# Optimization experiments

Measured on AMD Instinct MI355X. Metric: run time of the kernel, lower is better.

The kernel has to match this reference:

```python
import jax, jax.numpy as jnp
import numpy as np

NEG_SLOPE = 0.2

def _gat_conv(x, src, dst, W, a_src, a_dst, b, heads, out_ch, concat):
    N = x.shape[0]
    h = (x @ W).reshape(N, heads, out_ch)                      # [N,H,C]
    al_s = jnp.einsum('nhc,hc->nh', h, a_src)                  # [N,H]
    al_d = jnp.einsum('nhc,hc->nh', h, a_dst)
    e = jax.nn.leaky_relu(al_s[src] + al_d[dst], NEG_SLOPE)    # [E,H]
    emax = jax.ops.segment_max(e, dst, num_segments=N)         # [N,H]
    ex = jnp.exp(e - emax[dst])
    denom = jax.ops.segment_sum(ex, dst, num_segments=N)
    alpha = ex / denom[dst]                                    # [E,H]
    msg = h[src] * alpha[:, :, None]                           # [E,H,C]
    out = jax.ops.segment_sum(msg, dst, num_segments=N)        # [N,H,C]
    if concat:
        out = out.reshape(N, heads * out_ch)
    else:
        out = out.mean(axis=1)
    return out + b

def _add_self_loops(edge_index, N):
    loops = jnp.arange(N, dtype=edge_index.dtype)
    src = jnp.concatenate([edge_index[0], loops])
    dst = jnp.concatenate([edge_index[1], loops])
    return src, dst

def setup_inputs() -> dict:
    key = jax.random.key(0)
    ks = jax.random.split(key, 16)
    N, E, Fin, C, H, G, OUT = 50000, 1600000, 128, 32, 8, 256, 64
    s = 0.05
    inp = {
        'x': jax.random.normal(ks[0], (N, Fin), jnp.float32),
        'edge_index': jax.random.randint(ks[1], (2, E), 0, N, jnp.int64),
        'batch': jnp.sort(jax.random.randint(ks[2], (N,), 0, G, jnp.int64)),
        'W0': jax.random.normal(ks[3], (Fin, H * C), jnp.float32) * s,
        'a_src0': jax.random.normal(ks[4], (H, C), jnp.float32) * s,
        'a_dst0': jax.random.normal(ks[5], (H, C), jnp.float32) * s,
        'b0': jnp.zeros((H * C,), jnp.float32),
        'W1': jax.random.normal(ks[6], (H * C, H * C), jnp.float32) * s,
        'a_src1': jax.random.normal(ks[7], (H, C), jnp.float32) * s,
        'a_dst1': jax.random.normal(ks[8], (H, C), jnp.float32) * s,
        'b1': jnp.zeros((H * C,), jnp.float32),
        'W2': jax.random.normal(ks[9], (H * C, C), jnp.float32) * s,
        'a_src2': jax.random.normal(ks[10], (1, C), jnp.float32) * s,
        'a_dst2': jax.random.normal(ks[11], (1, C), jnp.float32) * s,
        'b2': jnp.zeros((C,), jnp.float32),
        'lin_w': jax.random.normal(ks[12], (C, OUT), jnp.float32) * s,
        'lin_b': jnp.zeros((OUT,), jnp.float32),
    }
    return inp

def reference(x, edge_index, batch, W0, a_src0, a_dst0, b0, W1, a_src1, a_dst1, b1,
              W2, a_src2, a_dst2, b2, lin_w, lin_b):
    N = x.shape[0]
    G = 256
    src, dst = _add_self_loops(edge_index, N)
    h = jax.nn.relu(_gat_conv(x, src, dst, W0, a_src0, a_dst0, b0, 8, 32, True))
    h = jax.nn.relu(_gat_conv(h, src, dst, W1, a_src1, a_dst1, b1, 8, 32, True))
    h = _gat_conv(h, src, dst, W2, a_src2, a_dst2, b2, 1, 32, True)  # heads=1 concat -> [N,32]
    # global mean pool over graphs
    sums = jax.ops.segment_sum(h, batch, num_segments=G)
    cnts = jax.ops.segment_sum(jnp.ones((N,), h.dtype), batch, num_segments=G)
    pooled = sums / jnp.maximum(cnts, 1.0)[:, None]
    return pooled @ lin_w + lin_b
```

## Files before the change

kernel.cpp:

```cpp
#include <hip/hip_runtime.h>
#include <hip/hip_bf16.h>


#define LRELU(x) ((x) >= 0.f ? (x) : 0.2f * (x))

typedef unsigned short ushort8 __attribute__((ext_vector_type(8)));
typedef unsigned short ushort4v __attribute__((ext_vector_type(4)));
typedef __attribute__((ext_vector_type(8))) short bf16x8;
typedef __attribute__((ext_vector_type(4))) float f32x4;

__device__ __forceinline__ float bf2f(unsigned short u) {
    return __uint_as_float(((unsigned)u) << 16);
}
__device__ __forceinline__ unsigned short f2bf(float f) {
    __hip_bfloat16 b = __float2bfloat16(f);
    return *reinterpret_cast<unsigned short*>(&b);
}
__device__ __forceinline__ void gl_lds16(const unsigned short* g, unsigned short* l) {
    __builtin_amdgcn_global_load_lds((const __attribute__((address_space(1))) void*)g,
                                     (__attribute__((address_space(3))) void*)l, 16, 0, 0);
}


template <int BM, int BN, int WM, int WN, int H>
__device__ __forceinline__
void gemm_core(unsigned short* __restrict__ Ab, unsigned short* __restrict__ Bb,
               const unsigned short* __restrict__ A, const unsigned short* __restrict__ Bt,
               unsigned short* __restrict__ Cc,
               const float* __restrict__ a_src, const float* __restrict__ a_dst,
               float* __restrict__ als, float* __restrict__ ald,
               int M, int Nn, int K, int bxi, int byi) {
    constexpr int BK = 64;
    constexpr int MT = WM / 16, NT = WN / 16;
    constexpr int NWX = BN / WN;
    constexpr int NHL = WN / 32;
    const int tid = threadIdx.x;
    const int lane = tid & 63;
    const int wave = tid >> 6;
    const int wx = wave % NWX, wy = wave / NWX;
    const int by = byi * BM;
    const int bx = bxi * BN;
    const int r16 = lane & 15, kg = lane >> 4;
    const int srow = lane >> 3, sslot = lane & 7;

    f32x4 acc[MT][NT];
#pragma unroll
    for (int i = 0; i < MT; i++)
#pragma unroll
        for (int j = 0; j < NT; j++) acc[i][j] = (f32x4){0.f, 0.f, 0.f, 0.f};

    for (int k0 = 0; k0 < K; k0 += BK) {
        for (int t = wave; t < BM / 8; t += 4) {
            int gm = by + t * 8 + srow;
            if (gm >= M) gm = M - 1;
            gl_lds16(A + (size_t)gm * K + k0 + sslot * 8, Ab + (t * 8) * BK);
        }
        for (int t = wave; t < BN / 8; t += 4) {
            int gn = bx + t * 8 + srow;
            gl_lds16(Bt + (size_t)gn * K + k0 + sslot * 8, Bb + (t * 8) * BK);
        }
        __syncthreads();
#pragma unroll
        for (int ks = 0; ks < 2; ks++) {
            bf16x8 bh[NT];
#pragma unroll
            for (int j = 0; j < NT; j++)
                bh[j] = *(const bf16x8*)(Bb + (wx * WN + j * 16 + r16) * BK + ks * 32 + kg * 8);
#pragma unroll
            for (int i = 0; i < MT; i++) {
                bf16x8 ah = *(const bf16x8*)(Ab + (wy * WM + i * 16 + r16) * BK + ks * 32 + kg * 8);
#pragma unroll
                for (int j = 0; j < NT; j++)
                    acc[i][j] = __builtin_amdgcn_mfma_f32_16x16x32_bf16(ah, bh[j], acc[i][j], 0, 0, 0);
            }
        }
        __syncthreads();
    }

    const int c0 = bx + wx * WN;
#pragma unroll
    for (int i = 0; i < MT; i++) {
#pragma unroll
        for (int r = 0; r < 4; r++) {
            int gm = by + wy * WM + i * 16 + kg * 4 + r;
            bool ok = gm < M;
            float sa[NHL] = {};
            float sd[NHL] = {};
#pragma unroll
            for (int j = 0; j < NT; j++) {
                int gn = c0 + j * 16 + r16;
                float v = acc[i][j][r];
                if (ok) Cc[(size_t)gm * Nn + gn] = f2bf(v);
                sa[j >> 1] += v * a_src[gn];
                sd[j >> 1] += v * a_dst[gn];
            }
#pragma unroll
            for (int m = 1; m < 16; m <<= 1) {
#pragma unroll
                for (int t = 0; t < NHL; t++) {
                    sa[t] += __shfl_xor(sa[t], m);
                    sd[t] += __shfl_xor(sd[t], m);
                }
            }
            if (ok && r16 == 0) {
#pragma unroll
                for (int t = 0; t < NHL; t++) {
                    int hh = (c0 >> 5) + t;
                    als[(size_t)gm * H + hh] = sa[t];
                    ald[(size_t)gm * H + hh] = sd[t];
                }
            }
        }
    }
}


__global__ __launch_bounds__(256)
void deg_prep_kernel(const int* __restrict__ dst, int* __restrict__ deg, int E, int N,
                     const float* __restrict__ x, const float* __restrict__ W0,
                     const float* __restrict__ W1, const float* __restrict__ W2,
                     unsigned short* __restrict__ xb, unsigned short* __restrict__ w0t,
                     unsigned short* __restrict__ w1t, unsigned short* __restrict__ w2t,
                     int DEG_BLKS) {
    if ((int)blockIdx.x < DEG_BLKS) {
        int i = blockIdx.x * 256 + threadIdx.x;
        if (i < E) atomicAdd(&deg[dst[i]], 1);
        else if (i < E + N) atomicAdd(&deg[i - E], 1);
        return;
    }
    int i = (blockIdx.x - DEG_BLKS) * 256 + threadIdx.x;
    int nx = N * 128;
    if (i < nx) { xb[i] = f2bf(x[i]); return; }
    i -= nx;
    if (i < 256 * 128) {
        int n = i / 128, k = i - n * 128;
        w0t[i] = f2bf(W0[(size_t)k * 256 + n]);
        return;
    }
    i -= 256 * 128;
    if (i < 256 * 256) {
        int n = i / 256, k = i - n * 256;
        w1t[i] = f2bf(W1[(size_t)k * 256 + n]);
        return;
    }
    i -= 256 * 256;
    if (i < 32 * 256) {
        int n = i / 256, k = i - n * 256;
        w2t[i] = f2bf(W2[(size_t)k * 32 + n]);
    }
}


__global__ void scan_kernel(const int* __restrict__ deg, int* __restrict__ rowptr, int n,
                            const int* __restrict__ batch, int* __restrict__ gstart,
                            int N, int G) {
    const int tid = threadIdx.x;
    if (tid <= G) {
        int lo = 0, hi = N;
        while (lo < hi) { int mid = (lo + hi) >> 1; if (batch[mid] < tid) lo = mid + 1; else hi = mid; }
        gstart[tid] = lo;
    }
    __shared__ int partial[1024];
    const int chunk = (n + 1023) / 1024;
    const int start = min(tid * chunk, n);
    const int end = min(start + chunk, n);
    int s = 0;
    for (int i = start; i < end; i++) s += deg[i];
    partial[tid] = s;
    __syncthreads();
    for (int o = 1; o < 1024; o <<= 1) {
        int v = (tid >= o) ? partial[tid - o] : 0;
        __syncthreads();
        partial[tid] += v;
        __syncthreads();
    }
    int run = (tid == 0) ? 0 : partial[tid - 1];
    for (int i = start; i < end; i++) { rowptr[i] = run; run += deg[i]; }
    if (tid == 0) rowptr[n] = partial[1023];
}


__global__ __launch_bounds__(256)
void mega0_kernel(const unsigned short* __restrict__ A, const unsigned short* __restrict__ Bt,
                  unsigned short* __restrict__ Cc,
                  const float* __restrict__ a_src, const float* __restrict__ a_dst,
                  float* __restrict__ als, float* __restrict__ ald, int M, int K,
                  const int* __restrict__ src, const int* __restrict__ dst,
                  int* __restrict__ rowptr, int* __restrict__ col, int E, int N,
                  int GEMM_BLKS, int SCAT_BLKS) {
    __shared__ __attribute__((aligned(16))) unsigned short Ab[128 * 64];
    __shared__ __attribute__((aligned(16))) unsigned short Bb[128 * 64];
    const int bid = blockIdx.x;
    if (bid < GEMM_BLKS) {
        gemm_core<128, 128, 64, 64, 8>(Ab, Bb, A, Bt, Cc, a_src, a_dst, als, ald,
                                       M, 256, K, bid & 1, bid >> 1);
        return;
    }
    const int sb = bid - GEMM_BLKS;
    const int bin = sb / SCAT_BLKS;
    const int i = (sb - bin * SCAT_BLKS) * 256 + threadIdx.x;
    const int lo = (int)((long long)N * bin / 4);
    const int hi = (int)((long long)N * (bin + 1) / 4);
    int s, d;
    if (i < E) { d = dst[i]; s = src[i]; }
    else if (i < E + N) { d = i - E; s = d; }
    else return;
    if (d < lo || d >= hi) return;
    int pos = atomicAdd(&rowptr[d], 1);
    col[pos] = s;
}


template <int BM, int BN, int WM, int WN, int H>
__global__ __launch_bounds__(256)
void gemm_bf16_al(const unsigned short* __restrict__ A, const unsigned short* __restrict__ Bt,
                  unsigned short* __restrict__ Cc,
                  const float* __restrict__ a_src, const float* __restrict__ a_dst,
                  float* __restrict__ als, float* __restrict__ ald,
                  int M, int Nn, int K) {
    __shared__ __attribute__((aligned(16))) unsigned short Ab[BM * 64];
    __shared__ __attribute__((aligned(16))) unsigned short Bb[BN * 64];
    gemm_core<BM, BN, WM, WN, H>(Ab, Bb, A, Bt, Cc, a_src, a_dst, als, ald,
                                 M, Nn, K, blockIdx.x, blockIdx.y);
}


__global__ __launch_bounds__(256)
void gat_agg_w8(const unsigned short* __restrict__ hfeat,
                const float* __restrict__ als, const float* __restrict__ ald,
                const int* __restrict__ rowptr,
                const int* __restrict__ col,
                const float* __restrict__ bias,
                unsigned short* __restrict__ outH,
                int N) {
    constexpr int CAP = 128;
    const int wid = threadIdx.x >> 6;
    const int lane = threadIdx.x & 63;
    const int n = blockIdx.x * 4 + wid;
    __shared__ float se_all[4][CAP * 8];
    __shared__ int scol_all[4][CAP];
    if (n >= N) return;
    float* se = se_all[wid];
    int* scol = scol_all[wid];

    const int r0 = (n == 0) ? 0 : rowptr[n - 1];
    const int deg = rowptr[n] - r0;
    const int dcap = min(deg, CAP);

    for (int j = lane; j < dcap; j += 64) scol[j] = col[r0 + j];

    const int slot = lane >> 3, h = lane & 7;
    const float aldh = ald[(size_t)n * 8 + h];
    float psum = 0.f;
    for (int j = 0; j < deg; j += 8) {
        int e = j + slot;
        if (e < deg) {
            int s = (e < dcap) ? scol[e] : col[r0 + e];
            float ev = als[(size_t)s * 8 + h] + aldh;
            ev = LRELU(ev);
            float w = __expf(ev);
            psum += w;
            if (e < CAP) se[e * 8 + h] = w;
        }
    }
#pragma unroll
    for (int m = 8; m < 64; m <<= 1) psum += __shfl_xor(psum, m);
    const int q = lane >> 3;
    const float sinv = 1.0f / __shfl(psum, q);
    const float aldq = ald[(size_t)n * 8 + q];

    const int cb = lane * 4;
    float a0 = 0.f, a1 = 0.f, a2 = 0.f, a3 = 0.f;
    int j = 0;
    for (; j + 3 < dcap; j += 4) {
        int s0 = __builtin_amdgcn_readfirstlane(scol[j]);
        int s1 = __builtin_amdgcn_readfirstlane(scol[j + 1]);
        int s2 = __builtin_amdgcn_readfirstlane(scol[j + 2]);
        int s3 = __builtin_amdgcn_readfirstlane(scol[j + 3]);
        ushort4v v0 = *(const ushort4v*)(hfeat + (size_t)s0 * 256 + cb);
        ushort4v v1 = *(const ushort4v*)(hfeat + (size_t)s1 * 256 + cb);
        ushort4v v2 = *(const ushort4v*)(hfeat + (size_t)s2 * 256 + cb);
        ushort4v v3 = *(const ushort4v*)(hfeat + (size_t)s3 * 256 + cb);
        float w0 = se[j * 8 + q];
        float w1 = se[j * 8 + 8 + q];
        float w2 = se[j * 8 + 16 + q];
        float w3 = se[j * 8 + 24 + q];
        a0 += bf2f(v0[0]) * w0; a1 += bf2f(v0[1]) * w0; a2 += bf2f(v0[2]) * w0; a3 += bf2f(v0[3]) * w0;
        a0 += bf2f(v1[0]) * w1; a1 += bf2f(v1[1]) * w1; a2 += bf2f(v1[2]) * w1; a3 += bf2f(v1[3]) * w1;
        a0 += bf2f(v2[0]) * w2; a1 += bf2f(v2[1]) * w2; a2 += bf2f(v2[2]) * w2; a3 += bf2f(v2[3]) * w2;
        a0 += bf2f(v3[0]) * w3; a1 += bf2f(v3[1]) * w3; a2 += bf2f(v3[2]) * w3; a3 += bf2f(v3[3]) * w3;
    }
    for (; j < dcap; j++) {
        int s0 = __builtin_amdgcn_readfirstlane(scol[j]);
        ushort4v v0 = *(const ushort4v*)(hfeat + (size_t)s0 * 256 + cb);
        float w0 = se[j * 8 + q];
        a0 += bf2f(v0[0]) * w0; a1 += bf2f(v0[1]) * w0; a2 += bf2f(v0[2]) * w0; a3 += bf2f(v0[3]) * w0;
    }
    for (; j < deg; j++) {
        int s0 = col[r0 + j];
        float ev = als[(size_t)s0 * 8 + q] + aldq;
        ev = LRELU(ev);
        float w0 = __expf(ev);
        ushort4v v0 = *(const ushort4v*)(hfeat + (size_t)s0 * 256 + cb);
        a0 += bf2f(v0[0]) * w0; a1 += bf2f(v0[1]) * w0; a2 += bf2f(v0[2]) * w0; a3 += bf2f(v0[3]) * w0;
    }

    float4 b4 = *(const float4*)&bias[cb];
    float o0 = fmaxf(a0 * sinv + b4.x, 0.f);
    float o1 = fmaxf(a1 * sinv + b4.y, 0.f);
    float o2 = fmaxf(a2 * sinv + b4.z, 0.f);
    float o3 = fmaxf(a3 * sinv + b4.w, 0.f);
    const size_t ob = (size_t)n * 256 + cb;
    *(ushort4v*)&outH[ob] = (ushort4v){f2bf(o0), f2bf(o1), f2bf(o2), f2bf(o3)};
}


__global__ __launch_bounds__(256)
void gat_agg_h1w(const unsigned short* __restrict__ hfeat,
                 const float* __restrict__ als, const float* __restrict__ ald,
                 const int* __restrict__ rowptr, const int* __restrict__ col,
                 const float* __restrict__ bias, float* __restrict__ out, int N) {
    constexpr int CAP = 256;
    const int wid = threadIdx.x >> 6;
    const int lane = threadIdx.x & 63;
    const int n = blockIdx.x * 4 + wid;
    __shared__ float sw_all[4][CAP];
    __shared__ int scol_all[4][CAP];
    if (n >= N) return;
    float* sw = sw_all[wid];
    int* scol = scol_all[wid];

    const int r0 = (n == 0) ? 0 : rowptr[n - 1];
    const int deg = rowptr[n] - r0;
    const int dcap = min(deg, CAP);
    const float aldn = ald[n];

    float lsum = 0.f;
    for (int idx = lane; idx < deg; idx += 64) {
        int s = col[r0 + idx];
        float ev = als[s] + aldn;
        ev = LRELU(ev);
        float w = __expf(ev);
        if (idx < CAP) { sw[idx] = w; scol[idx] = s; }
        lsum += w;
    }
#pragma unroll
    for (int m = 1; m < 64; m <<= 1) lsum += __shfl_xor(lsum, m);
    const float sinv = 1.0f / lsum;

    const int slot = lane >> 3, ch = lane & 7;
    float a0 = 0.f, a1 = 0.f, a2 = 0.f, a3 = 0.f;
    for (int j = 0; j < dcap; j += 8) {
        int e = j + slot;
        int ec = min(e, dcap - 1);
        int s = scol[ec];
        float w = (e < dcap) ? sw[ec] : 0.f;
        ushort4v v = *(const ushort4v*)(hfeat + (size_t)s * 32 + ch * 4);
        a0 += bf2f(v[0]) * w; a1 += bf2f(v[1]) * w;
        a2 += bf2f(v[2]) * w; a3 += bf2f(v[3]) * w;
    }
    for (int j = CAP; j < deg; j += 8) {
        int e = j + slot;
        int ec = min(e, deg - 1);
        int s = col[r0 + ec];
        float w = 0.f;
        if (e < deg) {
            float ev = als[s] + aldn;
            ev = LRELU(ev);
            w = __expf(ev);
        }
        ushort4v v = *(const ushort4v*)(hfeat + (size_t)s * 32 + ch * 4);
        a0 += bf2f(v[0]) * w; a1 += bf2f(v[1]) * w;
        a2 += bf2f(v[2]) * w; a3 += bf2f(v[3]) * w;
    }
#pragma unroll
    for (int m = 8; m < 64; m <<= 1) {
        a0 += __shfl_xor(a0, m);
        a1 += __shfl_xor(a1, m);
        a2 += __shfl_xor(a2, m);
        a3 += __shfl_xor(a3, m);
    }
    if (slot == 0) {
        float4 b4 = *(const float4*)&bias[ch * 4];
        float4 o;
        o.x = a0 * sinv + b4.x;
        o.y = a1 * sinv + b4.y;
        o.z = a2 * sinv + b4.z;
        o.w = a3 * sinv + b4.w;
        *(float4*)&out[(size_t)n * 32 + ch * 4] = o;
    }
}


__global__ __launch_bounds__(256)
void pool_final_kernel(const float* __restrict__ h, const int* __restrict__ gstart,
                       const float* __restrict__ lin_w, const float* __restrict__ lin_b,
                       float* __restrict__ out) {
    const int g = blockIdx.x;
    const int tid = threadIdx.x;
    const int n0 = gstart[g], n1 = gstart[g + 1];
    const int r = tid >> 5, c = tid & 31;
    __shared__ float pp[4][32];
    __shared__ float pm[32];
    float acc = 0.f;
    for (int n = n0 + r; n < n1; n += 8) acc += h[(size_t)n * 32 + c];
    acc += __shfl_xor(acc, 32);
    if ((tid & 63) < 32) pp[tid >> 6][c] = acc;
    __syncthreads();
    if (tid < 32) {
        float s = pp[0][tid] + pp[1][tid] + pp[2][tid] + pp[3][tid];
        pm[tid] = s / fmaxf((float)(n1 - n0), 1.f);
    }
    __syncthreads();
    if (tid < 64) {
        float a = lin_b[tid];
#pragma unroll 8
        for (int cc = 0; cc < 32; cc++) a += pm[cc] * lin_w[cc * 64 + tid];
        out[(size_t)g * 64 + tid] = a;
    }
}


extern "C" void kernel_launch(void* const* d_in, const int* in_sizes, int n_in,
                              void* d_out, int out_size, void* d_ws, size_t ws_size,
                              hipStream_t stream) {
    const float* x     = (const float*)d_in[0];
    const int*   ei    = (const int*)d_in[1];
    const int*   batch = (const int*)d_in[2];
    const float* W0    = (const float*)d_in[3];
    const float* a_s0  = (const float*)d_in[4];
    const float* a_d0  = (const float*)d_in[5];
    const float* b0    = (const float*)d_in[6];
    const float* W1    = (const float*)d_in[7];
    const float* a_s1  = (const float*)d_in[8];
    const float* a_d1  = (const float*)d_in[9];
    const float* b1    = (const float*)d_in[10];
    const float* W2    = (const float*)d_in[11];
    const float* a_s2  = (const float*)d_in[12];
    const float* a_d2  = (const float*)d_in[13];
    const float* b2    = (const float*)d_in[14];
    const float* lin_w = (const float*)d_in[15];
    const float* lin_b = (const float*)d_in[16];

    const int N = in_sizes[0] / 128;
    const int E = in_sizes[1] / 2;
    const int G = 256;
    const int Etot = E + N;
    const int* src = ei;
    const int* dst = ei + E;

    char* w = (char*)d_ws;
    size_t off = 0;
    auto alloc = [&](size_t bytes) -> void* {
        void* p = (void*)(w + off);
        off += (bytes + 255) & ~(size_t)255;
        return p;
    };
    int* deg    = (int*)alloc((size_t)N * 4);
    int* rowptr = (int*)alloc((size_t)(N + 1) * 4);
    int* colA   = (int*)alloc((size_t)Etot * 4);
    int* gstart = (int*)alloc((size_t)(G + 1) * 4);
    float* als  = (float*)alloc((size_t)N * 8 * 4);
    float* ald  = (float*)alloc((size_t)N * 8 * 4);
    unsigned short* hb  = (unsigned short*)alloc((size_t)N * 256 * 2);
    unsigned short* g0  = (unsigned short*)alloc((size_t)N * 256 * 2);
    float* out2 = (float*)alloc((size_t)N * 32 * 4);
    unsigned short* w0t = (unsigned short*)alloc((size_t)256 * 128 * 2);
    unsigned short* w1t = (unsigned short*)alloc((size_t)256 * 256 * 2);
    unsigned short* w2t = (unsigned short*)alloc((size_t)32 * 256 * 2);
    unsigned short* xb = g0;

    hipMemsetAsync(deg, 0, (size_t)N * 4, stream);

    {
        const int DEG_BLKS = (Etot + 255) / 256;
        long long prep_elems = (long long)N * 128 + 256 * 128 + 256 * 256 + 32 * 256;
        const int PREP_BLKS = (int)((prep_elems + 255) / 256);
        deg_prep_kernel<<<DEG_BLKS + PREP_BLKS, 256, 0, stream>>>(
            dst, deg, E, N, x, W0, W1, W2, xb, w0t, w1t, w2t, DEG_BLKS);
    }

    scan_kernel<<<1, 1024, 0, stream>>>(deg, rowptr, N, batch, gstart, N, G);

    const int MB = (N + 127) / 128;

    {
        const int GEMM_BLKS = 2 * MB;
        const int SCAT_BLKS = (Etot + 255) / 256;
        mega0_kernel<<<GEMM_BLKS + 4 * SCAT_BLKS, 256, 0, stream>>>(
            xb, w0t, hb, a_s0, a_d0, als, ald, N, 128,
            src, dst, rowptr, colA, E, N, GEMM_BLKS, SCAT_BLKS);
    }
    gat_agg_w8<<<(N + 3) / 4, 256, 0, stream>>>(hb, als, ald, rowptr, colA, b0, g0, N);

    gemm_bf16_al<128, 128, 64, 64, 8><<<dim3(2, MB), 256, 0, stream>>>(
        g0, w1t, hb, a_s1, a_d1, als, ald, N, 256, 256);
    gat_agg_w8<<<(N + 3) / 4, 256, 0, stream>>>(hb, als, ald, rowptr, colA, b1, g0, N);

    gemm_bf16_al<128, 32, 32, 32, 1><<<dim3(1, MB), 256, 0, stream>>>(
        g0, w2t, hb, a_s2, a_d2, als, ald, N, 32, 256);
    gat_agg_h1w<<<(N + 3) / 4, 256, 0, stream>>>(hb, als, ald, rowptr, colA, b2, out2, N);

    pool_final_kernel<<<G, 256, 0, stream>>>(out2, gstart, lin_w, lin_b, (float*)d_out);
}
```

Baseline: 581.4 us.

## Fuse scan into degree kernel, pool via atomics, halve scatter bins

```diff
diff --git a/kernel.cpp b/kernel.cpp
--- a/kernel.cpp
+++ b/kernel.cpp
@@ -116,19 +116,51 @@
 
 
 __global__ __launch_bounds__(256)
-void deg_prep_kernel(const int* __restrict__ dst, int* __restrict__ deg, int E, int N,
-                     const float* __restrict__ x, const float* __restrict__ W0,
-                     const float* __restrict__ W1, const float* __restrict__ W2,
-                     unsigned short* __restrict__ xb, unsigned short* __restrict__ w0t,
-                     unsigned short* __restrict__ w1t, unsigned short* __restrict__ w2t,
-                     int DEG_BLKS) {
+void deg_prep_scan(const int* __restrict__ dst, int* __restrict__ deg, int E, int N,
+                   const float* __restrict__ x, const float* __restrict__ W0,
+                   const float* __restrict__ W1, const float* __restrict__ W2,
+                   unsigned short* __restrict__ xb, unsigned short* __restrict__ w0t,
+                   unsigned short* __restrict__ w1t, unsigned short* __restrict__ w2t,
+                   int DEG_BLKS, int* __restrict__ done,
+                   int* __restrict__ rowptr, const int* __restrict__ batch,
+                   int* __restrict__ gstart, int G) {
+    const int tid = threadIdx.x;
     if ((int)blockIdx.x < DEG_BLKS) {
-        int i = blockIdx.x * 256 + threadIdx.x;
+        int i = blockIdx.x * 256 + tid;
         if (i < E) atomicAdd(&deg[dst[i]], 1);
         else if (i < E + N) atomicAdd(&deg[i - E], 1);
+        __shared__ int islast;
+        __threadfence();
+        __syncthreads();
+        if (tid == 0) islast = (atomicAdd(done, 1) == DEG_BLKS - 1);
+        __syncthreads();
+        if (!islast) return;
+        __threadfence();
+        for (int g = tid; g <= G; g += 256) {
+            int lo = 0, hi = N;
+            while (lo < hi) { int mid = (lo + hi) >> 1; if (batch[mid] < g) lo = mid + 1; else hi = mid; }
+            gstart[g] = lo;
+        }
+        __shared__ int partial[256];
+        const int chunk = (N + 255) / 256;
+        const int start = min(tid * chunk, N);
+        const int end = min(start + chunk, N);
+        int s = 0;
+        for (int i2 = start; i2 < end; i2++) s += deg[i2];
+        partial[tid] = s;
+        __syncthreads();
+        for (int o = 1; o < 256; o <<= 1) {
+            int v = (tid >= o) ? partial[tid - o] : 0;
+            __syncthreads();
+            partial[tid] += v;
+            __syncthreads();
+        }
+        int run = (tid == 0) ? 0 : partial[tid - 1];
+        for (int i2 = start; i2 < end; i2++) { rowptr[i2] = run; run += deg[i2]; }
+        if (tid == 0) rowptr[N] = partial[255];
         return;
     }
-    int i = (blockIdx.x - DEG_BLKS) * 256 + threadIdx.x;
+    int i = (blockIdx.x - DEG_BLKS) * 256 + tid;
     int nx = N * 128;
     if (i < nx) { xb[i] = f2bf(x[i]); return; }
     i -= nx;
@@ -148,35 +180,6 @@
         int n = i / 256, k = i - n * 256;
         w2t[i] = f2bf(W2[(size_t)k * 32 + n]);
     }
-}
-
-
-__global__ void scan_kernel(const int* __restrict__ deg, int* __restrict__ rowptr, int n,
-                            const int* __restrict__ batch, int* __restrict__ gstart,
-                            int N, int G) {
-    const int tid = threadIdx.x;
-    if (tid <= G) {
-        int lo = 0, hi = N;
-        while (lo < hi) { int mid = (lo + hi) >> 1; if (batch[mid] < tid) lo = mid + 1; else hi = mid; }
-        gstart[tid] = lo;
-    }
-    __shared__ int partial[1024];
-    const int chunk = (n + 1023) / 1024;
-    const int start = min(tid * chunk, n);
-    const int end = min(start + chunk, n);
-    int s = 0;
-    for (int i = start; i < end; i++) s += deg[i];
-    partial[tid] = s;
-    __syncthreads();
-    for (int o = 1; o < 1024; o <<= 1) {
-        int v = (tid >= o) ? partial[tid - o] : 0;
-        __syncthreads();
-        partial[tid] += v;
-        __syncthreads();
-    }
-    int run = (tid == 0) ? 0 : partial[tid - 1];
-    for (int i = start; i < end; i++) { rowptr[i] = run; run += deg[i]; }
-    if (tid == 0) rowptr[n] = partial[1023];
 }
 
 
@@ -199,8 +202,8 @@
     const int sb = bid - GEMM_BLKS;
     const int bin = sb / SCAT_BLKS;
     const int i = (sb - bin * SCAT_BLKS) * 256 + threadIdx.x;
-    const int lo = (int)((long long)N * bin / 4);
-    const int hi = (int)((long long)N * (bin + 1) / 4);
+    const int lo = (int)((long long)N * bin / 2);
+    const int hi = (int)((long long)N * (bin + 1) / 2);
     int s, d;
     if (i < E) { d = dst[i]; s = src[i]; }
     else if (i < E + N) { d = i - E; s = d; }
@@ -316,10 +319,11 @@
 
 
 __global__ __launch_bounds__(256)
-void gat_agg_h1w(const unsigned short* __restrict__ hfeat,
+void gat_agg_h1p(const unsigned short* __restrict__ hfeat,
                  const float* __restrict__ als, const float* __restrict__ ald,
                  const int* __restrict__ rowptr, const int* __restrict__ col,
-                 const float* __restrict__ bias, float* __restrict__ out, int N) {
+                 const float* __restrict__ bias, const int* __restrict__ batch,
+                 float* __restrict__ sums, int N) {
     constexpr int CAP = 256;
     const int wid = threadIdx.x >> 6;
     const int lane = threadIdx.x & 63;
@@ -382,42 +386,32 @@
     }
     if (slot == 0) {
         float4 b4 = *(const float4*)&bias[ch * 4];
-        float4 o;
-        o.x = a0 * sinv + b4.x;
-        o.y = a1 * sinv + b4.y;
-        o.z = a2 * sinv + b4.z;
-        o.w = a3 * sinv + b4.w;
-        *(float4*)&out[(size_t)n * 32 + ch * 4] = o;
-    }
-}
-
-
-__global__ __launch_bounds__(256)
-void pool_final_kernel(const float* __restrict__ h, const int* __restrict__ gstart,
-                       const float* __restrict__ lin_w, const float* __restrict__ lin_b,
-                       float* __restrict__ out) {
+        int g = batch[n];
+        float* sp = &sums[(size_t)g * 32 + ch * 4];
+        atomicAdd(&sp[0], a0 * sinv + b4.x);
+        atomicAdd(&sp[1], a1 * sinv + b4.y);
+        atomicAdd(&sp[2], a2 * sinv + b4.z);
+        atomicAdd(&sp[3], a3 * sinv + b4.w);
+    }
+}
+
+
+__global__ __launch_bounds__(64)
+void head_kernel(const float* __restrict__ sums, const int* __restrict__ gstart,
+                 const float* __restrict__ lin_w, const float* __restrict__ lin_b,
+                 float* __restrict__ out) {
     const int g = blockIdx.x;
     const int tid = threadIdx.x;
-    const int n0 = gstart[g], n1 = gstart[g + 1];
-    const int r = tid >> 5, c = tid & 31;
-    __shared__ float pp[4][32];
     __shared__ float pm[32];
-    float acc = 0.f;
-    for (int n = n0 + r; n < n1; n += 8) acc += h[(size_t)n * 32 + c];
-    acc += __shfl_xor(acc, 32);
-    if ((tid & 63) < 32) pp[tid >> 6][c] = acc;
+    if (tid < 32) {
+        float cn = fmaxf((float)(gstart[g + 1] - gstart[g]), 1.f);
+        pm[tid] = sums[(size_t)g * 32 + tid] / cn;
+    }
     __syncthreads();
-    if (tid < 32) {
-        float s = pp[0][tid] + pp[1][tid] + pp[2][tid] + pp[3][tid];
-        pm[tid] = s / fmaxf((float)(n1 - n0), 1.f);
-    }
-    __syncthreads();
-    if (tid < 64) {
-        float a = lin_b[tid];
+    float a = lin_b[tid];
 #pragma unroll 8
-        for (int cc = 0; cc < 32; cc++) a += pm[cc] * lin_w[cc * 64 + tid];
-        out[(size_t)g * 64 + tid] = a;
-    }
+    for (int cc = 0; cc < 32; cc++) a += pm[cc] * lin_w[cc * 64 + tid];
+    out[(size_t)g * 64 + tid] = a;
 }
 
 
@@ -456,7 +450,11 @@
         off += (bytes + 255) & ~(size_t)255;
         return p;
     };
+    size_t zoff0 = off;
     int* deg    = (int*)alloc((size_t)N * 4);
+    int* done   = (int*)alloc(4);
+    float* sums = (float*)alloc((size_t)G * 32 * 4);
+    size_t zbytes = off - zoff0;
     int* rowptr = (int*)alloc((size_t)(N + 1) * 4);
     int* colA   = (int*)alloc((size_t)Etot * 4);
     int* gstart = (int*)alloc((size_t)(G + 1) * 4);
@@ -464,30 +462,28 @@
     float* ald  = (float*)alloc((size_t)N * 8 * 4);
     unsigned short* hb  = (unsigned short*)alloc((size_t)N * 256 * 2);
     unsigned short* g0  = (unsigned short*)alloc((size_t)N * 256 * 2);
-    float* out2 = (float*)alloc((size_t)N * 32 * 4);
     unsigned short* w0t = (unsigned short*)alloc((size_t)256 * 128 * 2);
     unsigned short* w1t = (unsigned short*)alloc((size_t)256 * 256 * 2);
     unsigned short* w2t = (unsigned short*)alloc((size_t)32 * 256 * 2);
     unsigned short* xb = g0;
 
-    hipMemsetAsync(deg, 0, (size_t)N * 4, stream);
+    hipMemsetAsync((void*)(w + zoff0), 0, zbytes, stream);
 
     {
         const int DEG_BLKS = (Etot + 255) / 256;
         long long prep_elems = (long long)N * 128 + 256 * 128 + 256 * 256 + 32 * 256;
         const int PREP_BLKS = (int)((prep_elems + 255) / 256);
-        deg_prep_kernel<<<DEG_BLKS + PREP_BLKS, 256, 0, stream>>>(
-            dst, deg, E, N, x, W0, W1, W2, xb, w0t, w1t, w2t, DEG_BLKS);
-    }
-
-    scan_kernel<<<1, 1024, 0, stream>>>(deg, rowptr, N, batch, gstart, N, G);
+        deg_prep_scan<<<DEG_BLKS + PREP_BLKS, 256, 0, stream>>>(
+            dst, deg, E, N, x, W0, W1, W2, xb, w0t, w1t, w2t,
+            DEG_BLKS, done, rowptr, batch, gstart, G);
+    }
 
     const int MB = (N + 127) / 128;
 
     {
         const int GEMM_BLKS = 2 * MB;
         const int SCAT_BLKS = (Etot + 255) / 256;
-        mega0_kernel<<<GEMM_BLKS + 4 * SCAT_BLKS, 256, 0, stream>>>(
+        mega0_kernel<<<GEMM_BLKS + 2 * SCAT_BLKS, 256, 0, stream>>>(
             xb, w0t, hb, a_s0, a_d0, als, ald, N, 128,
             src, dst, rowptr, colA, E, N, GEMM_BLKS, SCAT_BLKS);
     }
@@ -499,7 +495,7 @@
 
     gemm_bf16_al<128, 32, 32, 32, 1><<<dim3(1, MB), 256, 0, stream>>>(
         g0, w2t, hb, a_s2, a_d2, als, ald, N, 32, 256);
-    gat_agg_h1w<<<(N + 3) / 4, 256, 0, stream>>>(hb, als, ald, rowptr, colA, b2, out2, N);
-
-    pool_final_kernel<<<G, 256, 0, stream>>>(out2, gstart, lin_w, lin_b, (float*)d_out);
-}
+    gat_agg_h1p<<<(N + 3) / 4, 256, 0, stream>>>(hb, als, ald, rowptr, colA, b2, batch, sums, N);
+
+    head_kernel<<<G, 64, 0, stream>>>(sums, gstart, lin_w, lin_b, (float*)d_out);
+}
```

Result: slower. 979.5 us (+68.5%).
